# Kernel optimization log

Measured on AMD Instinct MI355X. Metric: run time of the kernel, lower is better.

Reference implementation:

```python
import jax, jax.numpy as jnp
import numpy as np

COST_KEYPOINT = 1.0
COST_GIOU = 1.0


def box_cxcyczwhd_to_xyzxyz(b):
    c, s = b[..., :3], b[..., 3:]
    return jnp.concatenate([c - 0.5 * s, c + 0.5 * s], axis=-1)


def generalized_3d_box_iou(b1, b2):
    # b1: [N,6], b2: [M,6], both xyzxyz. Returns [N,M] GIoU.
    vol1 = jnp.prod(b1[:, 3:] - b1[:, :3], axis=-1)
    vol2 = jnp.prod(b2[:, 3:] - b2[:, :3], axis=-1)
    lt = jnp.maximum(b1[:, None, :3], b2[None, :, :3])
    rb = jnp.minimum(b1[:, None, 3:], b2[None, :, 3:])
    inter = jnp.prod(jnp.maximum(rb - lt, 0.0), axis=-1)
    union = vol1[:, None] + vol2[None, :] - inter
    iou = inter / union
    elt = jnp.minimum(b1[:, None, :3], b2[None, :, :3])
    erb = jnp.maximum(b1[:, None, 3:], b2[None, :, 3:])
    evol = jnp.prod(jnp.maximum(erb - elt, 0.0), axis=-1)
    return iou - (evol - union) / evol


@jax.jit
def compute_cost(pred_keypoints, pred_boxes, tgt_boxes, tgt_keypoints):
    bs, Q = pred_keypoints.shape[:2]
    out_kp = pred_keypoints.reshape(bs * Q, -1)            # [bs*Q, K*3]
    out_boxes = pred_boxes.reshape(bs * Q, 6)
    tgt_b = tgt_boxes.reshape(-1, 6)                        # [T_total, 6]
    tgt_kp = tgt_keypoints.reshape(tgt_b.shape[0], -1)      # [T_total, K*3]
    xyz_min = box_cxcyczwhd_to_xyzxyz(tgt_b)[:, :3]
    K3 = tgt_kp.shape[-1]
    kp = tgt_kp.reshape(-1, K3 // 3, 3)
    # normalize keypoints relative to box min-corner and box size
    dist_kp = ((kp - xyz_min[:, None, :]) / tgt_b[:, None, 3:]).reshape(-1, K3)
    # L1 cdist: [bs*Q, T_total]
    cost_kp = jnp.sum(jnp.abs(out_kp[:, None, :] - dist_kp[None, :, :]), axis=-1)
    cost_giou = -generalized_3d_box_iou(
        box_cxcyczwhd_to_xyzxyz(out_boxes), box_cxcyczwhd_to_xyzxyz(tgt_b))
    C = COST_KEYPOINT * cost_kp + COST_GIOU * cost_giou
    return C.reshape(bs, Q, -1)


def _lap(cost):
    # Jonker-Volgenant shortest-augmenting-path LAP (scipy-style).
    # cost: [n, m] with n <= m. Returns (arange(n), col4row).
    cost = np.asarray(cost, dtype=np.float64)
    n, m = cost.shape
    u = np.zeros(n)
    v = np.zeros(m)
    col4row = np.full(n, -1, np.int64)
    row4col = np.full(m, -1, np.int64)
    for curRow in range(n):
        path = np.full(m, -1, np.int64)
        SR = np.zeros(n, bool)
        SC = np.zeros(m, bool)
        shortest = np.full(m, np.inf)
        minVal = 0.0
        i = curRow
        sink = -1
        while sink == -1:
            SR[i] = True
            idx = np.where(~SC)[0]
            r = minVal + cost[i, idx] - u[i] - v[idx]
            better = r < shortest[idx]
            shortest[idx[better]] = r[better]
            path[idx[better]] = i
            jloc = np.argmin(shortest[idx])
            j = idx[jloc]
            minVal = shortest[j]
            SC[j] = True
            if row4col[j] == -1:
                sink = j
            else:
                i = row4col[j]
        u[curRow] += minVal
        mask = SR.copy()
        mask[curRow] = False
        u[mask] += minVal - shortest[col4row[mask]]
        v[SC] -= minVal - shortest[SC]
        j = sink
        while True:
            i = path[j]
            row4col[j] = i
            col4row[i], j = j, col4row[i]
            if i == curRow:
                break
    return np.arange(n), col4row


def _linear_sum_assignment(cost):
    # cost: [Q, T] with Q >= T; mirrors scipy's transpose handling:
    # returns (row_ind sorted ascending, matching col_ind).
    rows, cols = _lap(cost.T)  # rows = arange(T) targets, cols = query ids
    order = np.argsort(cols)
    return cols[order], rows[order]


def setup_inputs() -> dict:
    key = jax.random.key(0)
    k1, k2, k3, k4, k5, k6 = jax.random.split(key, 6)
    BS, Q, T, K = 16, 300, 50, 17
    pred_keypoints = jax.random.normal(k1, (BS, Q, K * 3), dtype=jnp.float32)
    pred_boxes = jnp.concatenate([
        jax.random.uniform(k2, (BS, Q, 3), dtype=jnp.float32),
        jax.random.uniform(k3, (BS, Q, 3), dtype=jnp.float32) * 0.5 + 0.05,
    ], axis=-1)
    tgt_boxes = jnp.concatenate([
        jax.random.uniform(k4, (BS, T, 3), dtype=jnp.float32),
        jax.random.uniform(k5, (BS, T, 3), dtype=jnp.float32) * 0.5 + 0.05,
    ], axis=-1)
    tgt_keypoints = jax.random.uniform(k6, (BS, T, K * 3), dtype=jnp.float32)
    return {"pred_keypoints": pred_keypoints, "pred_boxes": pred_boxes,
            "tgt_boxes": tgt_boxes, "tgt_keypoints": tgt_keypoints}


def reference(pred_keypoints, pred_boxes, tgt_boxes, tgt_keypoints):
    C = compute_cost(pred_keypoints, pred_boxes, tgt_boxes, tgt_keypoints)
    Cn = np.asarray(C)
    bs, Q, _ = Cn.shape
    T = tgt_boxes.shape[1]
    # per-image block of the column-split cost matrix, as in torch C.split(sizes, -1)
    idx = []
    for b in range(bs):
        i, j = _linear_sum_assignment(Cn[b, :, b * T:(b + 1) * T])
        idx.append(np.stack([i, j]))
    indices = jnp.asarray(np.stack(idx), dtype=jnp.int32)  # [bs, 2, T]
    return C, indices
```

## Files before the change

### kernel.cpp

```cpp
#include <hip/hip_runtime.h>
#include <math.h>

#define BSZ 16
#define NQ 300
#define NT 50
#define K3 51
#define NPRED (BSZ*NQ)
#define NTGT  (BSZ*NT)
#define NC    (NPRED*NTGT)
#define TSTRIDE 301
#define SMEMF 15104

template<int CTRL, int RMASK>
__device__ __forceinline__ double dpp_minstep_f64(double x) {
    long long bb = __double_as_longlong(x);
    int lo = (int)(bb & 0xFFFFFFFFll);
    int hi = (int)(bb >> 32);
    int mlo = __builtin_amdgcn_update_dpp(lo, lo, CTRL, RMASK, 0xF, false);
    int mhi = __builtin_amdgcn_update_dpp(hi, hi, CTRL, RMASK, 0xF, false);
    double other = __longlong_as_double(((long long)mhi << 32) | (long long)(unsigned)mlo);
    return fmin(x, other);
}
__device__ __forceinline__ double wave_min_f64(double x) {
    x = dpp_minstep_f64<0xB1, 0xF>(x);
    x = dpp_minstep_f64<0x4E, 0xF>(x);
    x = dpp_minstep_f64<0x141, 0xF>(x);
    x = dpp_minstep_f64<0x140, 0xF>(x);
    x = dpp_minstep_f64<0x142, 0xA>(x);
    x = dpp_minstep_f64<0x143, 0xC>(x);
    long long bb = __double_as_longlong(x);
    int lo = __builtin_amdgcn_readlane((int)(bb & 0xFFFFFFFFll), 63);
    int hi = __builtin_amdgcn_readlane((int)(bb >> 32), 63);
    return __longlong_as_double(((long long)hi << 32) | (long long)(unsigned)lo);
}
__device__ __forceinline__ double readlane_f64(double x, int lane) {
    long long bb = __double_as_longlong(x);
    int lo = __builtin_amdgcn_readlane((int)(bb & 0xFFFFFFFFll), lane);
    int hi = __builtin_amdgcn_readlane((int)(bb >> 32), lane);
    return __longlong_as_double(((long long)hi << 32) | (long long)(unsigned)lo);
}

__device__ __forceinline__ float giou_cost(
    float plt0, float plt1, float plt2, float prb0, float prb1, float prb2, float pvol,
    float tlt0, float tlt1, float tlt2, float trb0, float trb1, float trb2, float tvol)
{
    float inter = fmaxf(fminf(prb0,trb0) - fmaxf(plt0,tlt0), 0.f);
    inter *= fmaxf(fminf(prb1,trb1) - fmaxf(plt1,tlt1), 0.f);
    inter *= fmaxf(fminf(prb2,trb2) - fmaxf(plt2,tlt2), 0.f);
    float evol = fmaxf(fmaxf(prb0,trb0) - fminf(plt0,tlt0), 0.f);
    evol *= fmaxf(fmaxf(prb1,trb1) - fminf(plt1,tlt1), 0.f);
    evol *= fmaxf(fmaxf(prb2,trb2) - fminf(plt2,tlt2), 0.f);
    float uni = pvol + tvol - inter;
    return inter/uni - (evol - uni)/evol;
}

__global__ __launch_bounds__(1024) void fused_kernel(
    const float* __restrict__ pred_kp, const float* __restrict__ pred_boxes,
    const float* __restrict__ tgt_boxes, const float* __restrict__ tgt_kp,
    float* __restrict__ C, float* __restrict__ out_idx)
{
    __shared__ __align__(16) float smem[SMEMF];
    const int bid = blockIdx.x;
    const int tid = threadIdx.x;

    if (bid >= BSZ) {
        const int cb = bid - BSZ;
        const int pb = cb % 75, tb = cb / 75;
        const int p0 = pb * 64, t0 = tb * 80;
        float* s_dk   = smem;
        float* s_tbox = smem + 4480;
        float* s_pk   = smem + 5440;

        if (tid < 80) {
            const float* tb6 = tgt_boxes + (size_t)(t0 + tid) * 6;
            float c0=tb6[0], c1=tb6[1], c2=tb6[2], s0=tb6[3], s1=tb6[4], s2=tb6[5];
            float l0=c0-0.5f*s0, l1=c1-0.5f*s1, l2=c2-0.5f*s2;
            float r0=c0+0.5f*s0, r1=c1+0.5f*s1, r2=c2+0.5f*s2;
            float* tw = s_tbox + tid*12;
            tw[0]=l0; tw[1]=l1; tw[2]=l2; tw[3]=r0; tw[4]=r1; tw[5]=r2;
            tw[6]=(r0-l0)*(r1-l1)*(r2-l2);
            tw[9]=s0; tw[10]=s1; tw[11]=s2;
        }
        __syncthreads();
        for (int e = tid; e < 80*K3; e += 1024) {
            int t = e / K3; int c = e - t*K3; int d = c % 3;
            float kp = tgt_kp[(size_t)t0*K3 + e];
            s_dk[t*56 + c] = (kp - s_tbox[t*12 + d]) / s_tbox[t*12 + 9 + d];
        }
        for (int e = tid; e < 64*K3; e += 1024)
            s_pk[e] = pred_kp[(size_t)p0*K3 + e];
        __syncthreads();

        const int pl = tid & 63, g = tid >> 6;
        float a[K3];
        #pragma unroll
        for (int c = 0; c < K3; ++c) a[c] = s_pk[pl*K3 + c];
        const int p = p0 + pl;
        const float* pb6 = pred_boxes + (size_t)p * 6;
        float pc0=pb6[0],pc1=pb6[1],pc2=pb6[2],ps0=pb6[3],ps1=pb6[4],ps2=pb6[5];
        float plt0=pc0-0.5f*ps0, plt1=pc1-0.5f*ps1, plt2=pc2-0.5f*ps2;
        float prb0=pc0+0.5f*ps0, prb1=pc1+0.5f*ps1, prb2=pc2+0.5f*ps2;
        float pvol=(prb0-plt0)*(prb1-plt1)*(prb2-plt2);

        #pragma unroll
        for (int k = 0; k < 5; ++k) {
            int tl = g*5 + k;
            const float* bbp = s_dk + tl*56;
            float sum = 0.f;
            #pragma unroll
            for (int c4 = 0; c4 < 12; ++c4) {
                float4 q = *(const float4*)(bbp + 4*c4);
                sum += fabsf(a[4*c4+0] - q.x);
                sum += fabsf(a[4*c4+1] - q.y);
                sum += fabsf(a[4*c4+2] - q.z);
                sum += fabsf(a[4*c4+3] - q.w);
            }
            sum += fabsf(a[48] - bbp[48]);
            sum += fabsf(a[49] - bbp[49]);
            sum += fabsf(a[50] - bbp[50]);
            const float* tw = s_tbox + tl*12;
            float g_ = giou_cost(plt0,plt1,plt2,prb0,prb1,prb2,pvol,
                                 tw[0],tw[1],tw[2],tw[3],tw[4],tw[5],tw[6]);
            C[(size_t)p*NTGT + (t0+tl)] = sum - g_;
        }
        return;
    }

    const int b = bid;
    const int ln = tid & 63, w = tid >> 6;
    const int bq0 = b*NQ, bt0 = b*NT;
    float* tile = smem;

    for (int e = tid; e < NT*K3; e += 1024)
        tile[e] = tgt_kp[(size_t)bt0*K3 + e];
    __syncthreads();

    float dk[K3];
    float tl0=0,tl1=0,tl2=0,tr0=0,tr1=0,tr2=0,tvol=0;
    if (ln < NT) {
        const float* tb6 = tgt_boxes + (size_t)(bt0+ln)*6;
        float c0=tb6[0],c1=tb6[1],c2=tb6[2],s0=tb6[3],s1=tb6[4],s2=tb6[5];
        tl0=c0-0.5f*s0; tl1=c1-0.5f*s1; tl2=c2-0.5f*s2;
        tr0=c0+0.5f*s0; tr1=c1+0.5f*s1; tr2=c2+0.5f*s2;
        tvol=(tr0-tl0)*(tr1-tl1)*(tr2-tl2);
        #pragma unroll
        for (int c = 0; c < K3; ++c) {
            int d = c % 3;
            float L = (d==0)?tl0:((d==1)?tl1:tl2);
            float S = (d==0)?s0:((d==1)?s1:s2);
            dk[c] = (tile[ln*K3 + c] - L) / S;
        }
    }
    __syncthreads();

    for (int p = w; p < NQ; p += 16) {
        const float* prow = pred_kp + (size_t)(bq0+p)*K3;
        const float* pb6  = pred_boxes + (size_t)(bq0+p)*6;
        float pc0=pb6[0],pc1=pb6[1],pc2=pb6[2],ps0=pb6[3],ps1=pb6[4],ps2=pb6[5];
        float plt0=pc0-0.5f*ps0, plt1=pc1-0.5f*ps1, plt2=pc2-0.5f*ps2;
        float prb0=pc0+0.5f*ps0, prb1=pc1+0.5f*ps1, prb2=pc2+0.5f*ps2;
        float pvol=(prb0-plt0)*(prb1-plt1)*(prb2-plt2);
        if (ln < NT) {
            float sum = 0.f;
            #pragma unroll
            for (int c = 0; c < K3; ++c) sum += fabsf(prow[c] - dk[c]);
            float g_ = giou_cost(plt0,plt1,plt2,prb0,prb1,prb2,pvol,
                                 tl0,tl1,tl2,tr0,tr1,tr2,tvol);
            tile[ln*TSTRIDE + p] = sum - g_;
        }
    }
    __syncthreads();
    if (w != 0) return;

    double u = 0.0;
    int c4r = -1;
    double v[5], sh[5];
    int pth[5];
    #pragma unroll
    for (int s = 0; s < 5; ++s) v[s] = 0.0;
    const double DINF = __builtin_inf();

    for (int curRow = 0; curRow < NT; ++curRow) {
        #pragma unroll
        for (int s = 0; s < 5; ++s) { sh[s] = DINF; pth[s] = -1; }
        int SCm = (ln < 44) ? 0 : 0x10;
        unsigned long long SRmask = 0ull;
        int i = curRow;
        double minVal = 0.0;
        int sink = -1;

        while (true) {
            SRmask |= (1ull << i);
            float cf[5];
            #pragma unroll
            for (int s = 0; s < 5; ++s) cf[s] = tile[i*TSTRIDE + ln + 64*s];
            double u_i = readlane_f64(u, i);
            double lmin = DINF;
            #pragma unroll
            for (int s = 0; s < 5; ++s) {
                bool open = ((SCm >> s) & 1) == 0;
                double r = ((minVal + (double)cf[s]) - u_i) - v[s];
                bool upd = open && (r < sh[s]);
                sh[s]  = upd ? r : sh[s];
                pth[s] = upd ? i : pth[s];
                lmin = fmin(lmin, open ? sh[s] : DINF);
            }
            double m = wave_min_f64(lmin);
            minVal = m;
            unsigned long long b0 = __ballot((((SCm >> 0) & 1) == 0) && (sh[0] == m));
            unsigned long long b1 = __ballot((((SCm >> 1) & 1) == 0) && (sh[1] == m));
            unsigned long long b2 = __ballot((((SCm >> 2) & 1) == 0) && (sh[2] == m));
            unsigned long long b3 = __ballot((((SCm >> 3) & 1) == 0) && (sh[3] == m));
            unsigned long long b4 = __ballot((((SCm >> 4) & 1) == 0) && (sh[4] == m));
            int jstar;
            if      (b0) jstar =       __builtin_ctzll(b0);
            else if (b1) jstar =  64 + __builtin_ctzll(b1);
            else if (b2) jstar = 128 + __builtin_ctzll(b2);
            else if (b3) jstar = 192 + __builtin_ctzll(b3);
            else         jstar = 256 + __builtin_ctzll(b4);
            if (ln == (jstar & 63)) SCm |= 1 << (jstar >> 6);
            unsigned long long mm = __ballot((ln < NT) && (c4r == jstar));
            if (mm == 0ull) { sink = jstar; break; }
            i = __builtin_ctzll(mm);
        }

        int cg  = (c4r >= 0) ? c4r : 0;
        int gow = cg & 63, gsl = cg >> 6;
        double g0 = __shfl(sh[0], gow);
        double g1 = __shfl(sh[1], gow);
        double g2 = __shfl(sh[2], gow);
        double g3 = __shfl(sh[3], gow);
        double g4 = __shfl(sh[4], gow);
        double gg = g0;
        gg = (gsl == 1) ? g1 : gg;
        gg = (gsl == 2) ? g2 : gg;
        gg = (gsl == 3) ? g3 : gg;
        gg = (gsl == 4) ? g4 : gg;
        bool inSR = (ln < NT) && ((SRmask >> ln) & 1ull);
        double du = (ln == curRow) ? minVal : (minVal - gg);
        u = inSR ? (u + du) : u;
        #pragma unroll
        for (int s = 0; s < 5; ++s) {
            bool closed = ((SCm >> s) & 1) != 0;
            v[s] = closed ? (v[s] - (minVal - sh[s])) : v[s];
        }

        int j = sink;
        while (true) {
            int ow2 = j & 63, sl2 = j >> 6;
            int ps = pth[0];
            ps = (sl2==1) ? pth[1] : ps;
            ps = (sl2==2) ? pth[2] : ps;
            ps = (sl2==3) ? pth[3] : ps;
            ps = (sl2==4) ? pth[4] : ps;
            int ii = __builtin_amdgcn_readlane(ps, ow2);
            int jj = __builtin_amdgcn_readlane(c4r, ii);
            if (ln == ii) c4r = j;
            j = jj;
            if (ii == curRow) break;
        }
    }

    int* smem_i = (int*)smem;
    __threadfence_block();
    if (ln < NT) smem_i[ln] = c4r;
    __threadfence_block();
    int myc = c4r;
    int rank = 0;
    for (int s2 = 0; s2 < NT; ++s2) rank += (smem_i[s2] < myc) ? 1 : 0;
    if (ln < NT) {
        out_idx[b*(2*NT) + rank]      = (float)myc;
        out_idx[b*(2*NT) + NT + rank] = (float)ln;
    }
}

extern "C" void kernel_launch(void* const* d_in, const int* in_sizes, int n_in,
                              void* d_out, int out_size, void* d_ws, size_t ws_size,
                              hipStream_t stream)
{
    const float* pred_kp    = (const float*)d_in[0];
    const float* pred_boxes = (const float*)d_in[1];
    const float* tgt_boxes  = (const float*)d_in[2];
    const float* tgt_kp     = (const float*)d_in[3];
    float* C   = (float*)d_out;
    float* idx = C + NC;
    fused_kernel<<<dim3(BSZ + 750), 1024, 0, stream>>>(
        pred_kp, pred_boxes, tgt_boxes, tgt_kp, C, idx);
}
```

Measured before the change: 150.0 us.

## Split into cost and LAP kernels with register-resident cost rows and f32 min

The fused kernel becomes two launches. The cost kernel also writes the per-image diagonal block, transposed, into workspace. The LAP kernel runs as one 64-thread wave per image, holding its 50x300 cost slice in registers selected by a switch, which removes the separate per-image recomputation and the shared-memory reads. The wave minimum is first reduced in f32 and falls back to the f64 reduction only when the f32 minimum is not unique. The trade-offs are an extra launch, a global round-trip through workspace, and heavy register pressure in the LAP kernel that could cause spills.

```diff
diff --git a/kernel.cpp b/kernel.cpp
--- a/kernel.cpp
+++ b/kernel.cpp
@@ -8,8 +8,6 @@
 #define NPRED (BSZ*NQ)
 #define NTGT  (BSZ*NT)
 #define NC    (NPRED*NTGT)
-#define TSTRIDE 301
-#define SMEMF 15104
 
 template<int CTRL, int RMASK>
 __device__ __forceinline__ double dpp_minstep_f64(double x) {
@@ -33,6 +31,20 @@
     int hi = __builtin_amdgcn_readlane((int)(bb >> 32), 63);
     return __longlong_as_double(((long long)hi << 32) | (long long)(unsigned)lo);
 }
+template<int CTRL, int RMASK>
+__device__ __forceinline__ float dpp_minstep_f32(float x) {
+    int m = __builtin_amdgcn_update_dpp(__float_as_int(x), __float_as_int(x), CTRL, RMASK, 0xF, false);
+    return fminf(x, __int_as_float(m));
+}
+__device__ __forceinline__ float wave_min_f32(float x) {
+    x = dpp_minstep_f32<0xB1, 0xF>(x);
+    x = dpp_minstep_f32<0x4E, 0xF>(x);
+    x = dpp_minstep_f32<0x141, 0xF>(x);
+    x = dpp_minstep_f32<0x140, 0xF>(x);
+    x = dpp_minstep_f32<0x142, 0xA>(x);
+    x = dpp_minstep_f32<0x143, 0xC>(x);
+    return __int_as_float(__builtin_amdgcn_readlane(__float_as_int(x), 63));
+}
 __device__ __forceinline__ double readlane_f64(double x, int lane) {
     long long bb = __double_as_longlong(x);
     int lo = __builtin_amdgcn_readlane((int)(bb & 0xFFFFFFFFll), lane);
@@ -54,131 +66,107 @@
     return inter/uni - (evol - uni)/evol;
 }
 
-__global__ __launch_bounds__(1024) void fused_kernel(
+__global__ __launch_bounds__(1024) void cost_kernel(
     const float* __restrict__ pred_kp, const float* __restrict__ pred_boxes,
     const float* __restrict__ tgt_boxes, const float* __restrict__ tgt_kp,
-    float* __restrict__ C, float* __restrict__ out_idx)
-{
-    __shared__ __align__(16) float smem[SMEMF];
-    const int bid = blockIdx.x;
+    float* __restrict__ C, float* __restrict__ wsT)
+{
+    __shared__ __align__(16) float s_dk[80*56];
+    __shared__ float s_tbox[80*12];
+    __shared__ float s_pk[64*K3];
+
+    const int cb = blockIdx.x;
+    const int pb = cb % 75, tb = cb / 75;
+    const int p0 = pb * 64, t0 = tb * 80;
     const int tid = threadIdx.x;
 
-    if (bid >= BSZ) {
-        const int cb = bid - BSZ;
-        const int pb = cb % 75, tb = cb / 75;
-        const int p0 = pb * 64, t0 = tb * 80;
-        float* s_dk   = smem;
-        float* s_tbox = smem + 4480;
-        float* s_pk   = smem + 5440;
-
-        if (tid < 80) {
-            const float* tb6 = tgt_boxes + (size_t)(t0 + tid) * 6;
-            float c0=tb6[0], c1=tb6[1], c2=tb6[2], s0=tb6[3], s1=tb6[4], s2=tb6[5];
-            float l0=c0-0.5f*s0, l1=c1-0.5f*s1, l2=c2-0.5f*s2;
-            float r0=c0+0.5f*s0, r1=c1+0.5f*s1, r2=c2+0.5f*s2;
-            float* tw = s_tbox + tid*12;
-            tw[0]=l0; tw[1]=l1; tw[2]=l2; tw[3]=r0; tw[4]=r1; tw[5]=r2;
-            tw[6]=(r0-l0)*(r1-l1)*(r2-l2);
-            tw[9]=s0; tw[10]=s1; tw[11]=s2;
-        }
-        __syncthreads();
-        for (int e = tid; e < 80*K3; e += 1024) {
-            int t = e / K3; int c = e - t*K3; int d = c % 3;
-            float kp = tgt_kp[(size_t)t0*K3 + e];
-            s_dk[t*56 + c] = (kp - s_tbox[t*12 + d]) / s_tbox[t*12 + 9 + d];
-        }
-        for (int e = tid; e < 64*K3; e += 1024)
-            s_pk[e] = pred_kp[(size_t)p0*K3 + e];
-        __syncthreads();
-
-        const int pl = tid & 63, g = tid >> 6;
-        float a[K3];
+    if (tid < 80) {
+        const float* tb6 = tgt_boxes + (size_t)(t0 + tid) * 6;
+        float c0=tb6[0], c1=tb6[1], c2=tb6[2], s0=tb6[3], s1=tb6[4], s2=tb6[5];
+        float l0=c0-0.5f*s0, l1=c1-0.5f*s1, l2=c2-0.5f*s2;
+        float r0=c0+0.5f*s0, r1=c1+0.5f*s1, r2=c2+0.5f*s2;
+        float* tw = s_tbox + tid*12;
+        tw[0]=l0; tw[1]=l1; tw[2]=l2; tw[3]=r0; tw[4]=r1; tw[5]=r2;
+        tw[6]=(r0-l0)*(r1-l1)*(r2-l2);
+        tw[9]=s0; tw[10]=s1; tw[11]=s2;
+    }
+    __syncthreads();
+    for (int e = tid; e < 80*K3; e += 1024) {
+        int t = e / K3; int c = e - t*K3; int d = c % 3;
+        float kp = tgt_kp[(size_t)t0*K3 + e];
+        s_dk[t*56 + c] = (kp - s_tbox[t*12 + d]) / s_tbox[t*12 + 9 + d];
+    }
+    for (int e = tid; e < 64*K3; e += 1024)
+        s_pk[e] = pred_kp[(size_t)p0*K3 + e];
+    __syncthreads();
+
+    const int pl = tid & 63, g = tid >> 6;
+    float a[K3];
+    #pragma unroll
+    for (int c = 0; c < K3; ++c) a[c] = s_pk[pl*K3 + c];
+    const int p = p0 + pl;
+    const float* pb6 = pred_boxes + (size_t)p * 6;
+    float pc0=pb6[0],pc1=pb6[1],pc2=pb6[2],ps0=pb6[3],ps1=pb6[4],ps2=pb6[5];
+    float plt0=pc0-0.5f*ps0, plt1=pc1-0.5f*ps1, plt2=pc2-0.5f*ps2;
+    float prb0=pc0+0.5f*ps0, prb1=pc1+0.5f*ps1, prb2=pc2+0.5f*ps2;
+    float pvol=(prb0-plt0)*(prb1-plt1)*(prb2-plt2);
+    const int bb2  = p / NQ;
+    const int prel = p - bb2*NQ;
+
+    #pragma unroll
+    for (int k = 0; k < 5; ++k) {
+        int tl = g*5 + k;
+        const float* bbp = s_dk + tl*56;
+        float sum = 0.f;
         #pragma unroll
-        for (int c = 0; c < K3; ++c) a[c] = s_pk[pl*K3 + c];
-        const int p = p0 + pl;
-        const float* pb6 = pred_boxes + (size_t)p * 6;
-        float pc0=pb6[0],pc1=pb6[1],pc2=pb6[2],ps0=pb6[3],ps1=pb6[4],ps2=pb6[5];
-        float plt0=pc0-0.5f*ps0, plt1=pc1-0.5f*ps1, plt2=pc2-0.5f*ps2;
-        float prb0=pc0+0.5f*ps0, prb1=pc1+0.5f*ps1, prb2=pc2+0.5f*ps2;
-        float pvol=(prb0-plt0)*(prb1-plt1)*(prb2-plt2);
-
-        #pragma unroll
-        for (int k = 0; k < 5; ++k) {
-            int tl = g*5 + k;
-            const float* bbp = s_dk + tl*56;
-            float sum = 0.f;
-            #pragma unroll
-            for (int c4 = 0; c4 < 12; ++c4) {
-                float4 q = *(const float4*)(bbp + 4*c4);
-                sum += fabsf(a[4*c4+0] - q.x);
-                sum += fabsf(a[4*c4+1] - q.y);
-                sum += fabsf(a[4*c4+2] - q.z);
-                sum += fabsf(a[4*c4+3] - q.w);
-            }
-            sum += fabsf(a[48] - bbp[48]);
-            sum += fabsf(a[49] - bbp[49]);
-            sum += fabsf(a[50] - bbp[50]);
-            const float* tw = s_tbox + tl*12;
-            float g_ = giou_cost(plt0,plt1,plt2,prb0,prb1,prb2,pvol,
-                                 tw[0],tw[1],tw[2],tw[3],tw[4],tw[5],tw[6]);
-            C[(size_t)p*NTGT + (t0+tl)] = sum - g_;
-        }
-        return;
-    }
-
-    const int b = bid;
-    const int ln = tid & 63, w = tid >> 6;
-    const int bq0 = b*NQ, bt0 = b*NT;
-    float* tile = smem;
-
-    for (int e = tid; e < NT*K3; e += 1024)
-        tile[e] = tgt_kp[(size_t)bt0*K3 + e];
-    __syncthreads();
-
-    float dk[K3];
-    float tl0=0,tl1=0,tl2=0,tr0=0,tr1=0,tr2=0,tvol=0;
-    if (ln < NT) {
-        const float* tb6 = tgt_boxes + (size_t)(bt0+ln)*6;
-        float c0=tb6[0],c1=tb6[1],c2=tb6[2],s0=tb6[3],s1=tb6[4],s2=tb6[5];
-        tl0=c0-0.5f*s0; tl1=c1-0.5f*s1; tl2=c2-0.5f*s2;
-        tr0=c0+0.5f*s0; tr1=c1+0.5f*s1; tr2=c2+0.5f*s2;
-        tvol=(tr0-tl0)*(tr1-tl1)*(tr2-tl2);
-        #pragma unroll
-        for (int c = 0; c < K3; ++c) {
-            int d = c % 3;
-            float L = (d==0)?tl0:((d==1)?tl1:tl2);
-            float S = (d==0)?s0:((d==1)?s1:s2);
-            dk[c] = (tile[ln*K3 + c] - L) / S;
-        }
-    }
-    __syncthreads();
-
-    for (int p = w; p < NQ; p += 16) {
-        const float* prow = pred_kp + (size_t)(bq0+p)*K3;
-        const float* pb6  = pred_boxes + (size_t)(bq0+p)*6;
-        float pc0=pb6[0],pc1=pb6[1],pc2=pb6[2],ps0=pb6[3],ps1=pb6[4],ps2=pb6[5];
-        float plt0=pc0-0.5f*ps0, plt1=pc1-0.5f*ps1, plt2=pc2-0.5f*ps2;
-        float prb0=pc0+0.5f*ps0, prb1=pc1+0.5f*ps1, prb2=pc2+0.5f*ps2;
-        float pvol=(prb0-plt0)*(prb1-plt1)*(prb2-plt2);
-        if (ln < NT) {
-            float sum = 0.f;
-            #pragma unroll
-            for (int c = 0; c < K3; ++c) sum += fabsf(prow[c] - dk[c]);
-            float g_ = giou_cost(plt0,plt1,plt2,prb0,prb1,prb2,pvol,
-                                 tl0,tl1,tl2,tr0,tr1,tr2,tvol);
-            tile[ln*TSTRIDE + p] = sum - g_;
-        }
-    }
-    __syncthreads();
-    if (w != 0) return;
-
+        for (int c4 = 0; c4 < 12; ++c4) {
+            float4 q = *(const float4*)(bbp + 4*c4);
+            sum += fabsf(a[4*c4+0] - q.x);
+            sum += fabsf(a[4*c4+1] - q.y);
+            sum += fabsf(a[4*c4+2] - q.z);
+            sum += fabsf(a[4*c4+3] - q.w);
+        }
+        sum += fabsf(a[48] - bbp[48]);
+        sum += fabsf(a[49] - bbp[49]);
+        sum += fabsf(a[50] - bbp[50]);
+        const float* tw = s_tbox + tl*12;
+        float g_ = giou_cost(plt0,plt1,plt2,prb0,prb1,prb2,pvol,
+                             tw[0],tw[1],tw[2],tw[3],tw[4],tw[5],tw[6]);
+        float val = sum - g_;
+        C[(size_t)p*NTGT + (t0+tl)] = val;
+        int trel = (t0+tl) - bb2*NT;
+        if (trel >= 0 && trel < NT)
+            wsT[bb2*(NT*NQ) + trel*NQ + prel] = val;
+    }
+}
+
+__global__ __launch_bounds__(64) void lap_kernel(const float* __restrict__ wsT,
+                                                 float* __restrict__ out_idx)
+{
+    const int b  = blockIdx.x;
+    const int ln = threadIdx.x;
+    const float* gt = wsT + b*(NT*NQ);
+
+    float t0_[NT], t1_[NT], t2_[NT], t3_[NT], t4_[NT];
+    const int q4 = (ln < 44) ? (ln + 256) : 0;
+    #pragma unroll
+    for (int r = 0; r < NT; ++r) {
+        t0_[r] = gt[r*NQ + ln];
+        t1_[r] = gt[r*NQ + ln + 64];
+        t2_[r] = gt[r*NQ + ln + 128];
+        t3_[r] = gt[r*NQ + ln + 192];
+        t4_[r] = gt[r*NQ + q4];
+    }
+
+    const double DINF = __builtin_inf();
     double u = 0.0;
     int c4r = -1;
     double v[5], sh[5];
     int pth[5];
     #pragma unroll
     for (int s = 0; s < 5; ++s) v[s] = 0.0;
-    const double DINF = __builtin_inf();
+
+#define ROWC(I) case I: cfa[0]=t0_[I]; cfa[1]=t1_[I]; cfa[2]=t2_[I]; cfa[3]=t3_[I]; cfa[4]=t4_[I]; break;
 
     for (int curRow = 0; curRow < NT; ++curRow) {
         #pragma unroll
@@ -191,21 +179,37 @@
 
         while (true) {
             SRmask |= (1ull << i);
-            float cf[5];
-            #pragma unroll
-            for (int s = 0; s < 5; ++s) cf[s] = tile[i*TSTRIDE + ln + 64*s];
+            float cfa[5];
+            switch (i) {
+                ROWC(0)  ROWC(1)  ROWC(2)  ROWC(3)  ROWC(4)  ROWC(5)  ROWC(6)  ROWC(7)
+                ROWC(8)  ROWC(9)  ROWC(10) ROWC(11) ROWC(12) ROWC(13) ROWC(14) ROWC(15)
+                ROWC(16) ROWC(17) ROWC(18) ROWC(19) ROWC(20) ROWC(21) ROWC(22) ROWC(23)
+                ROWC(24) ROWC(25) ROWC(26) ROWC(27) ROWC(28) ROWC(29) ROWC(30) ROWC(31)
+                ROWC(32) ROWC(33) ROWC(34) ROWC(35) ROWC(36) ROWC(37) ROWC(38) ROWC(39)
+                ROWC(40) ROWC(41) ROWC(42) ROWC(43) ROWC(44) ROWC(45) ROWC(46) ROWC(47)
+                ROWC(48) ROWC(49)
+                default: cfa[0]=cfa[1]=cfa[2]=cfa[3]=cfa[4]=0.f; break;
+            }
             double u_i = readlane_f64(u, i);
             double lmin = DINF;
             #pragma unroll
             for (int s = 0; s < 5; ++s) {
                 bool open = ((SCm >> s) & 1) == 0;
-                double r = ((minVal + (double)cf[s]) - u_i) - v[s];
+                double r = ((minVal + (double)cfa[s]) - u_i) - v[s];
                 bool upd = open && (r < sh[s]);
                 sh[s]  = upd ? r : sh[s];
                 pth[s] = upd ? i : pth[s];
                 lmin = fmin(lmin, open ? sh[s] : DINF);
             }
-            double m = wave_min_f64(lmin);
+            float k32 = (float)lmin;
+            float m32 = wave_min_f32(k32);
+            unsigned long long candm = __ballot(k32 == m32);
+            double m;
+            if (__popcll(candm) == 1) {
+                m = readlane_f64(lmin, (int)__builtin_ctzll(candm));
+            } else {
+                m = wave_min_f64(lmin);
+            }
             minVal = m;
             unsigned long long b0 = __ballot((((SCm >> 0) & 1) == 0) && (sh[0] == m));
             unsigned long long b1 = __ballot((((SCm >> 1) & 1) == 0) && (sh[1] == m));
@@ -261,10 +265,9 @@
         }
     }
 
-    int* smem_i = (int*)smem;
-    __threadfence_block();
+    __shared__ int smem_i[NT];
     if (ln < NT) smem_i[ln] = c4r;
-    __threadfence_block();
+    __syncthreads();
     int myc = c4r;
     int rank = 0;
     for (int s2 = 0; s2 < NT; ++s2) rank += (smem_i[s2] < myc) ? 1 : 0;
@@ -284,6 +287,8 @@
     const float* tgt_kp     = (const float*)d_in[3];
     float* C   = (float*)d_out;
     float* idx = C + NC;
-    fused_kernel<<<dim3(BSZ + 750), 1024, 0, stream>>>(
-        pred_kp, pred_boxes, tgt_boxes, tgt_kp, C, idx);
-}
+    float* wsT = (float*)d_ws;
+
+    cost_kernel<<<750, 1024, 0, stream>>>(pred_kp, pred_boxes, tgt_boxes, tgt_kp, C, wsT);
+    lap_kernel<<<BSZ, 64, 0, stream>>>(wsT, idx);
+}
```

Measured after the change: 159.5 us. +6.3%, slower.
